# Kernel optimization log

Measured on AMD Instinct MI355X. Metric: run time of the kernel, lower is better.

## Reference

```python
import jax, jax.numpy as jnp
import numpy as np

B, S, D = 4, 4096, 256


def setup_inputs() -> dict:
    key = jax.random.key(0)
    ks = jax.random.split(key, 7)
    s = 1.0 / np.sqrt(D)
    return {
        "x": jax.random.normal(ks[0], (B, S, D), dtype=jnp.float32),
        "Wq": jax.random.uniform(ks[1], (D, D), jnp.float32, -s, s),
        "bq": jax.random.uniform(ks[2], (D,), jnp.float32, -s, s),
        "Wk": jax.random.uniform(ks[3], (D, D), jnp.float32, -s, s),
        "bk": jax.random.uniform(ks[4], (D,), jnp.float32, -s, s),
        "Wv": jax.random.uniform(ks[5], (D, D), jnp.float32, -s, s),
        "bv": jax.random.uniform(ks[6], (D,), jnp.float32, -s, s),
    }


def reference(x, Wq, bq, Wk, bk, Wv, bv):
    # nn.Linear: y = x @ W.T + b
    Q = jnp.einsum("bsd,ed->bse", x, Wq) + bq
    K = jnp.einsum("bsd,ed->bse", x, Wk) + bk
    V = jnp.einsum("bsd,ed->bse", x, Wv) + bv
    dk = Q.shape[-1]
    scores = jnp.einsum("bqd,bkd->bqk", Q, K) / jnp.sqrt(jnp.float32(dk))
    # NOTE: original applies softmax over dim=1 (the query axis), not -1.
    attn = jax.nn.softmax(scores, axis=1)
    out = jnp.einsum("bqk,bkd->bqd", attn, V)
    return out
```

## Files before the change

kernel.cpp:

```cpp
#include <hip/hip_runtime.h>

typedef short bf16x8 __attribute__((ext_vector_type(8)));
typedef float f32x4 __attribute__((ext_vector_type(4)));
typedef unsigned short u16;

#define S_LEN 4096
#define D_DIM 256
#define NROW  16384

__device__ __forceinline__ u16 f2bf(float f) {
    union { float f; unsigned u; } v; v.f = f;
    unsigned r = v.u + 0x7FFFu + ((v.u >> 16) & 1u);
    return (u16)(r >> 16);
}
__device__ __forceinline__ float bf2f(u16 h) {
    union { unsigned u; float f; } v; v.u = ((unsigned)h) << 16; return v.f;
}

__device__ __forceinline__ size_t fr_qk(int t, int kk) {
    return (size_t)t * 4096 + kk * 512;
}
__device__ __forceinline__ size_t fr_v(int p, int dt, int kk2) {
    return (size_t)p * 16384 + (dt * 2 + kk2) * 512;
}
__device__ __forceinline__ size_t e_base(int b, int kc, int qt) {
    return ((size_t)(b * 32768 + kc * 256 + qt)) * 512;
}

__device__ __forceinline__ void gll16(const u16* g, u16* l) {
    __builtin_amdgcn_global_load_lds(
        (const __attribute__((address_space(1))) unsigned int*)g,
        (__attribute__((address_space(3))) unsigned int*)l, 16, 0, 0);
}

#define WAITV4 asm volatile("s_waitcnt vmcnt(4)" ::: "memory")
#define WAITV2 asm volatile("s_waitcnt vmcnt(2)" ::: "memory")
#define WAITV0 asm volatile("s_waitcnt vmcnt(0)" ::: "memory")
#define WAITLGKM0 asm volatile("s_waitcnt lgkmcnt(0)" ::: "memory")
#define MEMFENCE asm volatile("" ::: "memory")

__global__ __launch_bounds__(256) void wconv(
    const float* __restrict__ Wq, const float* __restrict__ Wk,
    const float* __restrict__ Wv, u16* __restrict__ Wf)
{
    int i = blockIdx.x * 256 + threadIdx.x;
    int m = i >> 13;
    int idx = i & 8191;
    int ocol = idx >> 5;
    int d0 = (idx & 31) * 8;
    const float* s = (m == 0 ? Wq : (m == 1 ? Wk : Wv)) + ocol * 256 + d0;
    float4 v0 = *reinterpret_cast<const float4*>(s);
    float4 v1 = *reinterpret_cast<const float4*>(s + 4);
    union { ushort4 h[2]; int4 q; } t;
    t.h[0] = make_ushort4(f2bf(v0.x), f2bf(v0.y), f2bf(v0.z), f2bf(v0.w));
    t.h[1] = make_ushort4(f2bf(v1.x), f2bf(v1.y), f2bf(v1.z), f2bf(v1.w));
    size_t off = (size_t)m * 65536 + fr_qk(ocol >> 4, d0 >> 5)
               + ((d0 >> 3) & 3) * 128 + (ocol & 15) * 8;
    *reinterpret_cast<int4*>(Wf + off) = t.q;
}

__global__ __launch_bounds__(256) void qkv_proj(
    const float* __restrict__ x, const u16* __restrict__ Wf,
    const float* __restrict__ bq, const float* __restrict__ bk,
    const float* __restrict__ bv,
    u16* __restrict__ Qf, u16* __restrict__ Kf, u16* __restrict__ Vf)
{
    __shared__ u16 xs[32][264];
    const int tid = threadIdx.x;
    const int r0 = blockIdx.x * 32;

    #pragma unroll
    for (int i = 0; i < 8; ++i) {
        int c = i * 256 + tid;
        int row = c >> 6, c4 = c & 63;
        float4 v = reinterpret_cast<const float4*>(x + (size_t)(r0 + row) * D_DIM)[c4];
        *reinterpret_cast<ushort4*>(&xs[row][c4 * 4]) =
            make_ushort4(f2bf(v.x), f2bf(v.y), f2bf(v.z), f2bf(v.w));
    }
    __syncthreads();

    const int w = tid >> 6, l = tid & 63, lr = l & 15, lg = l >> 4;
    const int c0 = w * 64;

    bf16x8 a[2][8];
    #pragma unroll
    for (int qs = 0; qs < 2; ++qs)
        #pragma unroll
        for (int kk = 0; kk < 8; ++kk)
            a[qs][kk] = *reinterpret_cast<const bf16x8*>(&xs[qs * 16 + lr][kk * 32 + lg * 8]);

    const float* Bs[3] = {bq, bk, bv};

    #pragma unroll
    for (int m = 0; m < 3; ++m) {
        const u16* Wm = Wf + (size_t)m * 65536;
        f32x4 acc[2][4] = {};
        #pragma unroll
        for (int kk = 0; kk < 8; ++kk) {
            #pragma unroll
            for (int cf = 0; cf < 4; ++cf) {
                bf16x8 wfr = *reinterpret_cast<const bf16x8*>(
                    Wm + fr_qk(w * 4 + cf, kk) + l * 8);
                acc[0][cf] = __builtin_amdgcn_mfma_f32_16x16x32_bf16(a[0][kk], wfr, acc[0][cf], 0, 0, 0);
                acc[1][cf] = __builtin_amdgcn_mfma_f32_16x16x32_bf16(a[1][kk], wfr, acc[1][cf], 0, 0, 0);
            }
        }
        if (m < 2) {
            u16* outp = (m == 0) ? Qf : Kf;
            int t = r0 >> 4;
            #pragma unroll
            for (int qs = 0; qs < 2; ++qs) {
                #pragma unroll
                for (int cf = 0; cf < 4; ++cf) {
                    int col = c0 + cf * 16 + lr;
                    float bias = Bs[m][col];
                    size_t base = fr_qk(t + qs, col >> 5) + ((col >> 3) & 3) * 128 + (col & 7);
                    #pragma unroll
                    for (int r = 0; r < 4; ++r)
                        outp[base + (lg * 4 + r) * 8] = f2bf(acc[qs][cf][r] + bias);
                }
            }
        } else {
            int p  = (r0 >> 12) * 64 + ((r0 & 4095) >> 6);
            int kb = r0 & 63;
            #pragma unroll
            for (int qs = 0; qs < 2; ++qs) {
                #pragma unroll
                for (int cf = 0; cf < 4; ++cf) {
                    int d = c0 + cf * 16 + lr;
                    float bias = bv[d];
                    #pragma unroll
                    for (int r = 0; r < 4; ++r) {
                        int key = kb + qs * 16 + lg * 4 + r;
                        size_t off = fr_v(p, d >> 4, key >> 5)
                                   + ((key >> 3) & 3) * 128 + (d & 15) * 8 + (key & 7);
                        Vf[off] = f2bf(acc[qs][cf][r] + bias);
                    }
                }
            }
        }
    }
}

__global__ __launch_bounds__(256, 2) void score_exp(
    const u16* __restrict__ Qf, const u16* __restrict__ Kf,
    u16* __restrict__ Ef, float* __restrict__ Zp, int write_e)
{
    __shared__ __align__(16) u16 Qls[2][8192];
    const int tid = threadIdx.x, blk = blockIdx.x;
    const int xcd = blk & 7, sub = blk >> 3;
    const int b  = xcd >> 1;
    const int qq = ((xcd & 1) << 1) | (sub & 1);
    const int ktile = sub >> 1;
    const int w = tid >> 6, l = tid & 63, lr = l & 15, lg = l >> 4;
    const int k0 = ktile * 128;

    bf16x8 kreg[2][8];
    #pragma unroll
    for (int ks = 0; ks < 2; ++ks) {
        const int tk = b * 256 + (k0 >> 4) + w * 2 + ks;
        #pragma unroll
        for (int kk = 0; kk < 8; ++kk)
            kreg[ks][kk] = *reinterpret_cast<const bf16x8*>(Kf + fr_qk(tk, kk) + l * 8);
    }

    #define STAGE_Q(qt_, nb_) do { \
        const u16* g_ = Qf + ((size_t)(b * 256 + (qt_) * 2)) * 4096 + (w * 4) * 512 + l * 8; \
        u16* d_ = &Qls[nb_][(w * 4) * 512]; \
        _Pragma("unroll") \
        for (int f_ = 0; f_ < 4; ++f_) gll16(g_ + f_ * 512, d_ + f_ * 512); \
    } while (0)

    const int qt0 = qq * 32;
    STAGE_Q(qt0, 0);
    __syncthreads();

    float Z[2][4] = {};
    const float SC = 0.0625f;
    const int kc = ktile * 4 + w;

    for (int it = 0; it < 32; ++it) {
        const int cur = it & 1;
        if (it < 31) STAGE_Q(qt0 + it + 1, cur ^ 1);

        f32x4 acc[2][2] = {};
        #pragma unroll
        for (int kk = 0; kk < 8; ++kk) {
            #pragma unroll
            for (int qf = 0; qf < 2; ++qf) {
                bf16x8 qfr = *reinterpret_cast<const bf16x8*>(
                    &Qls[cur][(qf * 8 + kk) * 512 + l * 8]);
                acc[0][qf] = __builtin_amdgcn_mfma_f32_16x16x32_bf16(kreg[0][kk], qfr, acc[0][qf], 0, 0, 0);
                acc[1][qf] = __builtin_amdgcn_mfma_f32_16x16x32_bf16(kreg[1][kk], qfr, acc[1][qf], 0, 0, 0);
            }
        }
        #pragma unroll
        for (int ks = 0; ks < 2; ++ks) {
            #pragma unroll
            for (int qf = 0; qf < 2; ++qf) {
                float e0 = __expf(acc[ks][qf][0] * SC);
                float e1 = __expf(acc[ks][qf][1] * SC);
                float e2 = __expf(acc[ks][qf][2] * SC);
                float e3 = __expf(acc[ks][qf][3] * SC);
                Z[ks][0] += e0; Z[ks][1] += e1; Z[ks][2] += e2; Z[ks][3] += e3;
                if (write_e) {
                    size_t ad = e_base(b, kc, (qt0 + it) * 2 + qf)
                              + (ks * 2 + (lg >> 1)) * 128 + lr * 8 + (lg & 1) * 4;
                    *reinterpret_cast<ushort4*>(Ef + ad) =
                        make_ushort4(f2bf(e0), f2bf(e1), f2bf(e2), f2bf(e3));
                }
            }
        }
        __syncthreads();
    }

    #pragma unroll
    for (int ks = 0; ks < 2; ++ks) {
        #pragma unroll
        for (int r = 0; r < 4; ++r) {
            float z = Z[ks][r];
            z += __shfl_xor(z, 1);
            z += __shfl_xor(z, 2);
            z += __shfl_xor(z, 4);
            z += __shfl_xor(z, 8);
            if (lr == 0)
                Zp[qq * NROW + b * S_LEN + k0 + w * 32 + ks * 16 + lg * 4 + r] = z;
        }
    }
    #undef STAGE_Q
}

__global__ __launch_bounds__(256) void zrecip(
    const float* __restrict__ Zp, float* __restrict__ rZ)
{
    int i = blockIdx.x * 256 + threadIdx.x;
    rZ[i] = 1.0f / (((Zp[i] + Zp[NROW + i]) + Zp[2 * NROW + i]) + Zp[3 * NROW + i]);
}

__global__ __launch_bounds__(256) void zlog(
    const float* __restrict__ Zp, float* __restrict__ LZ)
{
    int i = blockIdx.x * 256 + threadIdx.x;
    LZ[i] = logf(((Zp[i] + Zp[NROW + i]) + Zp[2 * NROW + i]) + Zp[3 * NROW + i]);
}

__global__ __launch_bounds__(256) void vscale(
    u16* __restrict__ Vf, const float* __restrict__ rZ)
{
    int i = blockIdx.x * 256 + threadIdx.x;
    int frag = i >> 6, l8 = i & 63;
    int p = frag >> 5, sub = frag & 31, kk2 = sub & 1;
    int b = p >> 6, kt = p & 63;
    int kbase = b * S_LEN + kt * 64 + kk2 * 32 + (l8 >> 4) * 8;
    float4 rz0 = *reinterpret_cast<const float4*>(&rZ[kbase]);
    float4 rz1 = *reinterpret_cast<const float4*>(&rZ[kbase + 4]);
    ushort4* vp = reinterpret_cast<ushort4*>(Vf + (size_t)i * 8);
    ushort4 a = vp[0], c = vp[1];
    vp[0] = make_ushort4(f2bf(bf2f(a.x) * rz0.x), f2bf(bf2f(a.y) * rz0.y),
                         f2bf(bf2f(a.z) * rz0.z), f2bf(bf2f(a.w) * rz0.w));
    vp[1] = make_ushort4(f2bf(bf2f(c.x) * rz1.x), f2bf(bf2f(c.y) * rz1.y),
                         f2bf(bf2f(c.z) * rz1.z), f2bf(bf2f(c.w) * rz1.w));
}

__global__ __launch_bounds__(256, 4) void pv_gemm(
    const u16* __restrict__ Ef, const u16* __restrict__ Vf, float* __restrict__ out)
{
    __shared__ __align__(16) u16 Vls[2][8192];

    const int tid = threadIdx.x, blk = blockIdx.x;
    const int xcd = blk & 7, sub = blk >> 3;
    const int b  = xcd >> 1;
    const int ks = ((xcd & 1) << 1) | (sub & 1);
    const int qt64 = sub >> 1;
    const int w = tid >> 6, l = tid & 63, lr = l & 15, lg = l >> 4;
    const int qh = w & 1, dh = w >> 1;

    #define EADDR(it_, j_) \
        (Ef + e_base(b, ks * 32 + (it_), qt64 * 4 + qh * 2 + (j_)) + l * 8)

    #define STAGE_V(it_, nb_) do { \
        const int kc_ = ks * 32 + (it_); \
        const size_t vb_ = ((size_t)(b * 64 + (kc_ >> 1))) * 16384 + (kc_ & 1) * 512; \
        _Pragma("unroll") \
        for (int f_ = 0; f_ < 4; ++f_) { \
            int dt_ = w * 4 + f_; \
            gll16(Vf + vb_ + (size_t)(dt_ * 2) * 512 + l * 8, &Vls[nb_][dt_ * 512]); \
        } \
    } while (0)

    #define COMPUTE(nb_, e0_, e1_) do { \
        __builtin_amdgcn_s_setprio(1); \
        _Pragma("unroll") \
        for (int dt = 0; dt < 8; ++dt) { \
            bf16x8 vfr = *reinterpret_cast<const bf16x8*>( \
                &Vls[nb_][(dh * 8 + dt) * 512 + l * 8]); \
            acc[0][dt] = __builtin_amdgcn_mfma_f32_16x16x32_bf16(e0_, vfr, acc[0][dt], 0, 0, 0); \
            acc[1][dt] = __builtin_amdgcn_mfma_f32_16x16x32_bf16(e1_, vfr, acc[1][dt], 0, 0, 0); \
        } \
        __builtin_amdgcn_s_setprio(0); \
    } while (0)

    #define BODY(it_, eC0_, eC1_, eN0_, eN1_) do { \
        STAGE_V((it_) + 1, ((it_) + 1) & 1); \
        MEMFENCE; \
        eN0_ = *reinterpret_cast<const bf16x8*>(EADDR((it_) + 2, 0)); \
        eN1_ = *reinterpret_cast<const bf16x8*>(EADDR((it_) + 2, 1)); \
        MEMFENCE; \
        COMPUTE((it_) & 1, eC0_, eC1_); \
        WAITV2; \
        __builtin_amdgcn_s_barrier(); \
        MEMFENCE; \
    } while (0)

    f32x4 acc[2][8] = {};
    bf16x8 eA0, eA1, eB0, eB1, eC0, eC1;

    eA0 = *reinterpret_cast<const bf16x8*>(EADDR(0, 0));
    eA1 = *reinterpret_cast<const bf16x8*>(EADDR(0, 1));
    MEMFENCE;
    STAGE_V(0, 0);
    MEMFENCE;
    eB0 = *reinterpret_cast<const bf16x8*>(EADDR(1, 0));
    eB1 = *reinterpret_cast<const bf16x8*>(EADDR(1, 1));
    MEMFENCE;
    WAITV2;
    __builtin_amdgcn_s_barrier();
    MEMFENCE;

    #pragma unroll 1
    for (int base = 0; base < 30; base += 3) {
        BODY(base,     eA0, eA1, eC0, eC1);
        BODY(base + 1, eB0, eB1, eA0, eA1);
        BODY(base + 2, eC0, eC1, eB0, eB1);
    }
    STAGE_V(31, 1);
    COMPUTE(0, eA0, eA1);
    WAITV0;
    __builtin_amdgcn_s_barrier();
    MEMFENCE;
    COMPUTE(1, eB0, eB1);

    const int qg = b * S_LEN + qt64 * 64 + qh * 32;
    const int dg = dh * 128;
    #pragma unroll
    for (int qf = 0; qf < 2; ++qf) {
        #pragma unroll
        for (int dt = 0; dt < 8; ++dt) {
            #pragma unroll
            for (int r = 0; r < 4; ++r) {
                unsafeAtomicAdd(&out[(size_t)(qg + qf * 16 + lg * 4 + r) * D_DIM
                                     + dg + dt * 16 + lr],
                                acc[qf][dt][r]);
            }
        }
    }
    #undef EADDR
    #undef STAGE_V
    #undef COMPUTE
    #undef BODY
}

__global__ __launch_bounds__(512, 1) void attn_out_fb(
    const u16* __restrict__ Qf, const u16* __restrict__ Kf, const u16* __restrict__ Vf,
    const float* __restrict__ LZ, float* __restrict__ out)
{
    __shared__ __align__(16) u16 Kls[3][8192];
    __shared__ __align__(16) u16 Vls[4][8192];
    __shared__ __align__(16) u16 ps[8][2][1280];
    __shared__ __align__(16) float lzs[1024];

    const int tid = threadIdx.x, blk = blockIdx.x;
    const int xcd = blk & 7, sub = blk >> 3;
    const int b  = xcd >> 1;
    const int kq = ((xcd & 1) << 1) | (sub & 1);
    const int qtile = sub >> 1;
    const int w = tid >> 6, l = tid & 63, lr = l & 15, lg = l >> 4;
    const int q0 = qtile * 256 + w * 32;
    const int base_tk = b * 256;
    const int kt0 = kq * 32;

    bf16x8 qreg[2][8];
    #pragma unroll
    for (int qs = 0; qs < 2; ++qs) {
        const int tq = base_tk + ((q0 + qs * 16) >> 4);
        #pragma unroll
        for (int kk = 0; kk < 8; ++kk)
            qreg[qs][kk] = *reinterpret_cast<const bf16x8*>(Qf + fr_qk(tq, kk) + l * 8);
    }

    #define STAGE(kt_) do { \
        if (w < 4) { \
            const u16* g_ = Kf + ((size_t)(base_tk + (kt0 + (kt_)) * 2)) * 4096 + (w * 4) * 512 + l * 8; \
            u16* d_ = &Kls[(kt_) % 3][(w * 4) * 512]; \
            _Pragma("unroll") \
            for (int f_ = 0; f_ < 4; ++f_) gll16(g_ + f_ * 512, d_ + f_ * 512); \
        } else { \
            const int kta_ = kt0 + (kt_); \
            const size_t vb_ = ((size_t)(b * 64 + (kta_ >> 1))) * 16384 + (kta_ & 1) * 512; \
            const int dt0_ = (w - 4) * 4; \
            _Pragma("unroll") \
            for (int f_ = 0; f_ < 4; ++f_) \
                gll16(Vf + vb_ + (size_t)(dt0_ + f_) * 1024 + l * 8, &Vls[(kt_) % 4][(dt0_ + f_) * 512]); \
        } \
    } while (0)

    #define QK(kt_) do { \
        const u16* kb_ = &Kls[(kt_) % 3][0]; \
        __builtin_amdgcn_s_setprio(1); \
        _Pragma("unroll") \
        for (int kk = 0; kk < 8; ++kk) { \
            bf16x8 k0_ = *reinterpret_cast<const bf16x8*>(kb_ + kk * 512 + l * 8); \
            bf16x8 k1_ = *reinterpret_cast<const bf16x8*>(kb_ + (8 + kk) * 512 + l * 8); \
            sacc[0][0] = __builtin_amdgcn_mfma_f32_16x16x32_bf16(qreg[0][kk], k0_, sacc[0][0], 0, 0, 0); \
            sacc[0][1] = __builtin_amdgcn_mfma_f32_16x16x32_bf16(qreg[1][kk], k0_, sacc[0][1], 0, 0, 0); \
            sacc[1][0] = __builtin_amdgcn_mfma_f32_16x16x32_bf16(qreg[0][kk], k1_, sacc[1][0], 0, 0, 0); \
            sacc[1][1] = __builtin_amdgcn_mfma_f32_16x16x32_bf16(qreg[1][kk], k1_, sacc[1][1], 0, 0, 0); \
        } \
        __builtin_amdgcn_s_setprio(0); \
    } while (0)

    #define PV(j_) do { \
        const u16* vb_ = &Vls[(j_) % 4][0]; \
        const u16* pb_ = &ps[w][(j_) & 1][0]; \
        bf16x8 af0_ = *reinterpret_cast<const bf16x8*>(pb_ + lr * 40 + lg * 8); \
        bf16x8 af1_ = *reinterpret_cast<const bf16x8*>(pb_ + (16 + lr) * 40 + lg * 8); \
        __builtin_amdgcn_s_setprio(1); \
        _Pragma("unroll") \
        for (int dt = 0; dt < 16; ++dt) { \
            bf16x8 vf_ = *reinterpret_cast<const bf16x8*>(vb_ + dt * 512 + l * 8); \
            oacc[0][dt] = __builtin_amdgcn_mfma_f32_16x16x32_bf16(af0_, vf_, oacc[0][dt], 0, 0, 0); \
            oacc[1][dt] = __builtin_amdgcn_mfma_f32_16x16x32_bf16(af1_, vf_, oacc[1][dt], 0, 0, 0); \
        } \
        __builtin_amdgcn_s_setprio(0); \
    } while (0)

    #define SM(kt_) do { \
        u16* pw_ = &ps[w][(kt_) & 1][0]; \
        _Pragma("unroll") \
        for (int cf = 0; cf < 2; ++cf) { \
            float Lv_ = lzs[(kt_) * 32 + cf * 16 + lr]; \
            _Pragma("unroll") \
            for (int qs = 0; qs < 2; ++qs) \
                _Pragma("unroll") \
                for (int r = 0; r < 4; ++r) { \
                    float p_ = __expf(fmaf(sacc[cf][qs][r], SC, -Lv_)); \
                    pw_[(qs * 16 + lg * 4 + r) * 40 + cf * 16 + lr] = f2bf(p_); \
                } \
        } \
    } while (0)

    f32x4 oacc[2][16] = {};
    const float SC = 0.0625f;

    f32x4 lzv;
    if (tid < 256)
        lzv = *reinterpret_cast<const f32x4*>(LZ + b * S_LEN + kt0 * 32 + tid * 4);
    STAGE(0);
    STAGE(1);
    if (tid < 256)
        *reinterpret_cast<f32x4*>(&lzs[tid * 4]) = lzv;
    WAITLGKM0;
    WAITV4;
    __builtin_amdgcn_s_barrier();
    MEMFENCE;

    #pragma unroll 1
    for (int kt = 0; kt < 30; ++kt) {
        STAGE(kt + 2);
        f32x4 sacc[2][2] = {};
        QK(kt);
        if (kt > 0) PV(kt - 1);
        SM(kt);
        WAITV4;
        __builtin_amdgcn_s_barrier();
        MEMFENCE;
    }
    {
        f32x4 sacc[2][2] = {};
        QK(30); PV(29); SM(30);
        WAITV0;
        __builtin_amdgcn_s_barrier();
        MEMFENCE;
    }
    {
        f32x4 sacc[2][2] = {};
        QK(31); PV(30); SM(31); PV(31);
    }

    #pragma unroll
    for (int qs = 0; qs < 2; ++qs) {
        #pragma unroll
        for (int dt = 0; dt < 16; ++dt) {
            #pragma unroll
            for (int r = 0; r < 4; ++r) {
                int row = q0 + qs * 16 + lg * 4 + r;
                unsafeAtomicAdd(&out[((size_t)(b * S_LEN + row)) * D_DIM + dt * 16 + lr],
                                oacc[qs][dt][r]);
            }
        }
    }
    #undef STAGE
    #undef QK
    #undef PV
    #undef SM
}

extern "C" void kernel_launch(void* const* d_in, const int* in_sizes, int n_in,
                              void* d_out, int out_size, void* d_ws, size_t ws_size,
                              hipStream_t stream) {
    const float* x  = (const float*)d_in[0];
    const float* Wq = (const float*)d_in[1];
    const float* bq = (const float*)d_in[2];
    const float* Wk = (const float*)d_in[3];
    const float* bk = (const float*)d_in[4];
    const float* Wv = (const float*)d_in[5];
    const float* bv = (const float*)d_in[6];
    float* out = (float*)d_out;

    u16* Qf = (u16*)d_ws;
    u16* Kf = Qf + (size_t)NROW * D_DIM;
    u16* Vf = Kf + (size_t)NROW * D_DIM;
    u16* Wf = Vf + (size_t)NROW * D_DIM;
    float* Zp = (float*)(Wf + 196608);
    float* rZ = Zp + 4 * NROW;
    u16* Ef = (u16*)(rZ + NROW);

    const size_t need = (size_t)((char*)Ef - (char*)d_ws) + (size_t)4 * 32768 * 512 * 2;

    hipMemsetAsync(out, 0, (size_t)NROW * D_DIM * sizeof(float), stream);
    wconv<<<96, 256, 0, stream>>>(Wq, Wk, Wv, Wf);
    qkv_proj<<<NROW / 32, 256, 0, stream>>>(x, Wf, bq, bk, bv, Qf, Kf, Vf);

    if (ws_size >= need) {
        score_exp<<<512, 256, 0, stream>>>(Qf, Kf, Ef, Zp, 1);
        zrecip<<<NROW / 256, 256, 0, stream>>>(Zp, rZ);
        vscale<<<2048, 256, 0, stream>>>(Vf, rZ);
        pv_gemm<<<1024, 256, 0, stream>>>(Ef, Vf, out);
    } else {
        score_exp<<<512, 256, 0, stream>>>(Qf, Kf, Qf , Zp, 0);
        zlog<<<NROW / 256, 256, 0, stream>>>(Zp, rZ);
        attn_out_fb<<<256, 512, 0, stream>>>(Qf, Kf, Vf, rZ, out);
    }
}
```

Before: 164.5 us.

## Retile PV GEMM to 128x128 output tiles with finer key split

Result: slower. 241.5 us (+46.8%).

```diff
diff --git a/kernel.cpp b/kernel.cpp
--- a/kernel.cpp
+++ b/kernel.cpp
@@ -34,7 +34,6 @@
 }
 
 #define WAITV4 asm volatile("s_waitcnt vmcnt(4)" ::: "memory")
-#define WAITV2 asm volatile("s_waitcnt vmcnt(2)" ::: "memory")
 #define WAITV0 asm volatile("s_waitcnt vmcnt(0)" ::: "memory")
 #define WAITLGKM0 asm volatile("s_waitcnt lgkmcnt(0)" ::: "memory")
 #define MEMFENCE asm volatile("" ::: "memory")
@@ -265,97 +264,123 @@
 __global__ __launch_bounds__(256, 4) void pv_gemm(
     const u16* __restrict__ Ef, const u16* __restrict__ Vf, float* __restrict__ out)
 {
-    __shared__ __align__(16) u16 Vls[2][8192];
+    __shared__ __align__(16) u16 Vls[2][4096];
 
     const int tid = threadIdx.x, blk = blockIdx.x;
     const int xcd = blk & 7, sub = blk >> 3;
-    const int b  = xcd >> 1;
-    const int ks = ((xcd & 1) << 1) | (sub & 1);
-    const int qt64 = sub >> 1;
+    const int b   = xcd >> 1;
+    const int kq  = ((xcd & 1) << 2) | (sub & 3);
+    const int rem = sub >> 2;
+    const int qt  = rem >> 1;
+    const int dh2 = rem & 1;
     const int w = tid >> 6, l = tid & 63, lr = l & 15, lg = l >> 4;
     const int qh = w & 1, dh = w >> 1;
 
     #define EADDR(it_, j_) \
-        (Ef + e_base(b, ks * 32 + (it_), qt64 * 4 + qh * 2 + (j_)) + l * 8)
+        (Ef + e_base(b, kq * 16 + (it_), qt * 8 + qh * 4 + (j_)) + l * 8)
 
     #define STAGE_V(it_, nb_) do { \
-        const int kc_ = ks * 32 + (it_); \
+        const int kc_ = kq * 16 + (it_); \
         const size_t vb_ = ((size_t)(b * 64 + (kc_ >> 1))) * 16384 + (kc_ & 1) * 512; \
         _Pragma("unroll") \
-        for (int f_ = 0; f_ < 4; ++f_) { \
-            int dt_ = w * 4 + f_; \
-            gll16(Vf + vb_ + (size_t)(dt_ * 2) * 512 + l * 8, &Vls[nb_][dt_ * 512]); \
+        for (int f_ = 0; f_ < 2; ++f_) { \
+            int fl_ = w * 2 + f_; \
+            gll16(Vf + vb_ + (size_t)((dh2 * 8 + fl_) * 1024) + l * 8, &Vls[nb_][fl_ * 512]); \
         } \
     } while (0)
 
-    #define COMPUTE(nb_, e0_, e1_) do { \
+    #define LOADE(it_, e0_, e1_, e2_, e3_) do { \
+        e0_ = *reinterpret_cast<const bf16x8*>(EADDR(it_, 0)); \
+        e1_ = *reinterpret_cast<const bf16x8*>(EADDR(it_, 1)); \
+        e2_ = *reinterpret_cast<const bf16x8*>(EADDR(it_, 2)); \
+        e3_ = *reinterpret_cast<const bf16x8*>(EADDR(it_, 3)); \
+    } while (0)
+
+    #define COMPUTE(nb_, e0_, e1_, e2_, e3_) do { \
         __builtin_amdgcn_s_setprio(1); \
         _Pragma("unroll") \
-        for (int dt = 0; dt < 8; ++dt) { \
+        for (int df = 0; df < 4; ++df) { \
             bf16x8 vfr = *reinterpret_cast<const bf16x8*>( \
-                &Vls[nb_][(dh * 8 + dt) * 512 + l * 8]); \
-            acc[0][dt] = __builtin_amdgcn_mfma_f32_16x16x32_bf16(e0_, vfr, acc[0][dt], 0, 0, 0); \
-            acc[1][dt] = __builtin_amdgcn_mfma_f32_16x16x32_bf16(e1_, vfr, acc[1][dt], 0, 0, 0); \
+                &Vls[nb_][(dh * 4 + df) * 512 + l * 8]); \
+            acc[0][df] = __builtin_amdgcn_mfma_f32_16x16x32_bf16(e0_, vfr, acc[0][df], 0, 0, 0); \
+            acc[1][df] = __builtin_amdgcn_mfma_f32_16x16x32_bf16(e1_, vfr, acc[1][df], 0, 0, 0); \
+            acc[2][df] = __builtin_amdgcn_mfma_f32_16x16x32_bf16(e2_, vfr, acc[2][df], 0, 0, 0); \
+            acc[3][df] = __builtin_amdgcn_mfma_f32_16x16x32_bf16(e3_, vfr, acc[3][df], 0, 0, 0); \
         } \
         __builtin_amdgcn_s_setprio(0); \
     } while (0)
 
-    #define BODY(it_, eC0_, eC1_, eN0_, eN1_) do { \
+    #define BODY(it_, C0,C1,C2,C3, N0,N1,N2,N3) do { \
         STAGE_V((it_) + 1, ((it_) + 1) & 1); \
         MEMFENCE; \
-        eN0_ = *reinterpret_cast<const bf16x8*>(EADDR((it_) + 2, 0)); \
-        eN1_ = *reinterpret_cast<const bf16x8*>(EADDR((it_) + 2, 1)); \
+        LOADE((it_) + 2, N0, N1, N2, N3); \
         MEMFENCE; \
-        COMPUTE((it_) & 1, eC0_, eC1_); \
-        WAITV2; \
+        COMPUTE((it_) & 1, C0, C1, C2, C3); \
+        WAITV4; \
         __builtin_amdgcn_s_barrier(); \
         MEMFENCE; \
     } while (0)
 
-    f32x4 acc[2][8] = {};
-    bf16x8 eA0, eA1, eB0, eB1, eC0, eC1;
-
-    eA0 = *reinterpret_cast<const bf16x8*>(EADDR(0, 0));
-    eA1 = *reinterpret_cast<const bf16x8*>(EADDR(0, 1));
+    f32x4 acc[4][4] = {};
+    bf16x8 eA0, eA1, eA2, eA3, eB0, eB1, eB2, eB3, eC0, eC1, eC2, eC3;
+
+    LOADE(0, eA0, eA1, eA2, eA3);
     MEMFENCE;
     STAGE_V(0, 0);
     MEMFENCE;
-    eB0 = *reinterpret_cast<const bf16x8*>(EADDR(1, 0));
-    eB1 = *reinterpret_cast<const bf16x8*>(EADDR(1, 1));
-    MEMFENCE;
-    WAITV2;
+    LOADE(1, eB0, eB1, eB2, eB3);
+    MEMFENCE;
+    WAITV4;
     __builtin_amdgcn_s_barrier();
     MEMFENCE;
 
     #pragma unroll 1
-    for (int base = 0; base < 30; base += 3) {
-        BODY(base,     eA0, eA1, eC0, eC1);
-        BODY(base + 1, eB0, eB1, eA0, eA1);
-        BODY(base + 2, eC0, eC1, eB0, eB1);
-    }
-    STAGE_V(31, 1);
-    COMPUTE(0, eA0, eA1);
+    for (int base = 0; base < 12; base += 3) {
+        BODY(base,     eA0,eA1,eA2,eA3, eC0,eC1,eC2,eC3);
+        BODY(base + 1, eB0,eB1,eB2,eB3, eA0,eA1,eA2,eA3);
+        BODY(base + 2, eC0,eC1,eC2,eC3, eB0,eB1,eB2,eB3);
+    }
+    STAGE_V(13, 1);
+    MEMFENCE;
+    LOADE(14, eC0, eC1, eC2, eC3);
+    MEMFENCE;
+    COMPUTE(0, eA0, eA1, eA2, eA3);
+    WAITV4;
+    __builtin_amdgcn_s_barrier();
+    MEMFENCE;
+    STAGE_V(14, 0);
+    MEMFENCE;
+    LOADE(15, eA0, eA1, eA2, eA3);
+    MEMFENCE;
+    COMPUTE(1, eB0, eB1, eB2, eB3);
+    WAITV4;
+    __builtin_amdgcn_s_barrier();
+    MEMFENCE;
+    STAGE_V(15, 1);
+    MEMFENCE;
+    COMPUTE(0, eC0, eC1, eC2, eC3);
     WAITV0;
     __builtin_amdgcn_s_barrier();
     MEMFENCE;
-    COMPUTE(1, eB0, eB1);
-
-    const int qg = b * S_LEN + qt64 * 64 + qh * 32;
-    const int dg = dh * 128;
-    #pragma unroll
-    for (int qf = 0; qf < 2; ++qf) {
-        #pragma unroll
-        for (int dt = 0; dt < 8; ++dt) {
+    COMPUTE(1, eA0, eA1, eA2, eA3);
+
+    const int qg = b * S_LEN + qt * 128 + qh * 64;
+    const int dg = dh2 * 128 + dh * 64;
+    #pragma unroll
+    for (int qf = 0; qf < 4; ++qf) {
+        #pragma unroll
+        for (int df = 0; df < 4; ++df) {
             #pragma unroll
             for (int r = 0; r < 4; ++r) {
                 unsafeAtomicAdd(&out[(size_t)(qg + qf * 16 + lg * 4 + r) * D_DIM
-                                     + dg + dt * 16 + lr],
-                                acc[qf][dt][r]);
+                                     + dg + df * 16 + lr],
+                                acc[qf][df][r]);
             }
         }
     }
     #undef EADDR
     #undef STAGE_V
+    #undef LOADE
     #undef COMPUTE
     #undef BODY
 }
@@ -535,7 +560,7 @@
         score_exp<<<512, 256, 0, stream>>>(Qf, Kf, Ef, Zp, 1);
         zrecip<<<NROW / 256, 256, 0, stream>>>(Zp, rZ);
         vscale<<<2048, 256, 0, stream>>>(Vf, rZ);
-        pv_gemm<<<1024, 256, 0, stream>>>(Ef, Vf, out);
+        pv_gemm<<<2048, 256, 0, stream>>>(Ef, Vf, out);
     } else {
         score_exp<<<512, 256, 0, stream>>>(Qf, Kf, Qf , Zp, 0);
         zlog<<<NROW / 256, 256, 0, stream>>>(Zp, rZ);
```
